# Kernel optimization log

Hardware: AMD Instinct MI355X
Metric: run time of the kernel (lower is better)

## Reference

```python
import jax, jax.numpy as jnp
import numpy as np

GRID = 128
N_PTS = 60000
K = 27


def _occupied_coords():
    # Deterministic blob-like occupancy: top-N voxels of a smooth random field.
    rng = np.random.RandomState(0)
    xs = np.arange(GRID, dtype=np.float32)
    X, Y, Z = np.meshgrid(xs, xs, xs, indexing='ij')
    f = np.zeros((GRID, GRID, GRID), np.float32)
    for _ in range(12):
        k = rng.uniform(0.04, 0.22, 3).astype(np.float32)
        ph = np.float32(rng.uniform(0, 2 * np.pi))
        a = np.float32(rng.randn())
        f += a * np.cos(k[0] * X + k[1] * Y + k[2] * Z + ph)
    idx = np.argpartition(f.ravel(), -N_PTS)[-N_PTS:]
    return np.stack(np.unravel_index(idx, f.shape), axis=1).astype(np.int64)


def _keys(c):
    return (c[:, 0] * GRID + c[:, 1]) * GRID + c[:, 2]


def _build_kmap(coords):
    # ME-style kernel map: for each of 27 offsets, pairs (input_row, output_row)
    # such that coord[out] + offset == coord[in]. Padded with index n (dummy row).
    n = coords.shape[0]
    key = _keys(coords)
    order = np.argsort(key)
    skey = key[order]
    ins, outs = [], []
    for dx in (-1, 0, 1):
        for dy in (-1, 0, 1):
            for dz in (-1, 0, 1):
                q = coords + np.array([dx, dy, dz], dtype=np.int64)
                valid = np.all((q >= 0) & (q < GRID), axis=1)
                qk = _keys(q)
                pos = np.clip(np.searchsorted(skey, qk), 0, n - 1)
                hit = valid & (skey[pos] == qk)
                ins.append(order[pos[hit]].astype(np.int32))
                outs.append(np.nonzero(hit)[0].astype(np.int32))
    m = max(len(a) for a in ins)
    in_idx = np.full((K, m), n, np.int32)
    out_idx = np.full((K, m), n, np.int32)
    for k in range(K):
        in_idx[k, : len(ins[k])] = ins[k]
        out_idx[k, : len(outs[k])] = outs[k]
    return jnp.asarray(in_idx), jnp.asarray(out_idx)


def setup_inputs() -> dict:
    coords = _occupied_coords()
    in1, out1 = _build_kmap(coords)
    pc, parent = np.unique(coords // 2, axis=0, return_inverse=True)  # maxpool k2 s2
    in2, out2 = _build_kmap(pc)
    n_pool = int(pc.shape[0])
    ks = jax.random.split(jax.random.key(0), 12)
    f32 = jnp.float32
    feats = jax.random.normal(ks[0], (N_PTS, 128), f32)
    W1 = jax.random.normal(ks[1], (K, 128, 128), f32) / np.sqrt(128 * K)
    W2 = jax.random.normal(ks[2], (K, 128, 256), f32) / np.sqrt(128 * K)
    W3 = jax.random.normal(ks[3], (K, 256, 256), f32) / np.sqrt(256 * K)
    W4 = jax.random.normal(ks[4], (K, 256, 256), f32) / np.sqrt(256 * K)
    g1 = 1.0 + 0.1 * jax.random.normal(ks[5], (128,), f32)
    b1 = 0.1 * jax.random.normal(ks[6], (128,), f32)
    g2 = 1.0 + 0.1 * jax.random.normal(ks[7], (256,), f32)
    b2 = 0.1 * jax.random.normal(ks[8], (256,), f32)
    g3 = 1.0 + 0.1 * jax.random.normal(ks[9], (256,), f32)
    b3 = 0.1 * jax.random.normal(ks[10], (256,), f32)
    return dict(feats=feats, W1=W1, g1=g1, b1=b1, W2=W2, g2=g2, b2=b2,
                W3=W3, g3=g3, b3=b3, W4=W4,
                in1=in1, out1=out1, in2=in2, out2=out2,
                parent=jnp.asarray(parent.astype(np.int32)), n_pool=n_pool)


def _sparse_conv(x, in_idx, out_idx, W, n_out):
    # x: [N_in, Cin]; in_idx/out_idx: [K, M] padded with N_in / n_out; W: [K, Cin, Cout]
    xp = jnp.concatenate([x, jnp.zeros((1, x.shape[1]), x.dtype)], axis=0)
    acc0 = jnp.zeros((n_out + 1, W.shape[2]), x.dtype)

    def step(acc, xs):
        i, o, Wk = xs
        return acc.at[o].add(xp[i] @ Wk), None

    acc, _ = jax.lax.scan(step, acc0, (in_idx, out_idx, W))
    return acc[:-1]


def _bn_relu(x, g, b):
    # training-mode BatchNorm over active voxels (ME applies BatchNorm1d to features)
    m = x.mean(0)
    v = x.var(0)
    return jax.nn.relu((x - m) * jax.lax.rsqrt(v + 1e-5) * g + b)


def reference(feats, W1, g1, b1, W2, g2, b2, W3, g3, b3, W4,
              in1, out1, in2, out2, parent, n_pool):
    n = feats.shape[0]
    x = _bn_relu(_sparse_conv(feats, in1, out1, W1, n), g1, b1)          # [N,128]
    x = jax.ops.segment_max(x, parent, num_segments=n_pool)             # maxpool 2x2x2/2
    x = _bn_relu(_sparse_conv(x, in2, out2, W2, n_pool), g2, b2)         # [Np,256]
    x = _bn_relu(_sparse_conv(x, in2, out2, W3, n_pool), g3, b3)         # [Np,256]
    return _sparse_conv(x, in2, out2, W4, n_pool)                        # [Np,256]
```

## Files before the change

### kernel.cpp

```cpp
#include <hip/hip_runtime.h>
#include <hip/hip_bf16.h>
#include <math.h>

#define K_OFF 27

typedef __attribute__((ext_vector_type(8))) short short8v;
typedef __attribute__((ext_vector_type(4))) float float4v;

static __device__ __forceinline__ unsigned short f2bf(float f) {
  __hip_bfloat16 h = __float2bfloat16(f);
  return *reinterpret_cast<unsigned short*>(&h);
}

static __device__ __forceinline__ void gload_lds16(const void* g, void* l) {
  __builtin_amdgcn_global_load_lds(
      (const __attribute__((address_space(1))) void*)g,
      (__attribute__((address_space(3))) void*)l, 16, 0, 0);
}

__global__ void fill_i32_kernel(int* __restrict__ p, int total, int val) {
  int i = blockIdx.x * blockDim.x + threadIdx.x;
  if (i < total) p[i] = val;
}

__global__ void build_table_kernel(const int* __restrict__ in_idx,
                                   const int* __restrict__ out_idx,
                                   int* __restrict__ table, int M, int n_valid,
                                   int n_out_pad) {
  int j = blockIdx.x * blockDim.x + threadIdx.x;
  if (j >= K_OFF * M) return;
  int k = j / M;
  int in = in_idx[j], out = out_idx[j];
  if (in < n_valid && out < n_valid) table[k * n_out_pad + out] = in;
}

__global__ void wtrans_kernel(const float* __restrict__ W,
                              unsigned short* __restrict__ Wt, int Cin,
                              int Cout) {
  __shared__ float t[32][33];
  const int k = blockIdx.z, ci0 = blockIdx.x * 32, co0 = blockIdx.y * 32;
  const float* Wk = W + (size_t)k * Cin * Cout;
  unsigned short* Wtk = Wt + (size_t)k * Cout * Cin;
#pragma unroll
  for (int i = 0; i < 4; ++i)
    t[threadIdx.y + i * 8][threadIdx.x] =
        Wk[(size_t)(ci0 + threadIdx.y + i * 8) * Cout + co0 + threadIdx.x];
  __syncthreads();
#pragma unroll
  for (int i = 0; i < 4; ++i)
    Wtk[(size_t)(co0 + threadIdx.y + i * 8) * Cin + ci0 + threadIdx.x] =
        f2bf(t[threadIdx.x][threadIdx.y + i * 8]);
}

__global__ void f32_to_bf16_kernel(const float* __restrict__ s,
                                   unsigned short* __restrict__ d, int total) {
  int i = (blockIdx.x * blockDim.x + threadIdx.x) * 4;
  if (i >= total) return;
  float4 v = *reinterpret_cast<const float4*>(s + i);
  ushort4 o = {f2bf(v.x), f2bf(v.y), f2bf(v.z), f2bf(v.w)};
  *reinterpret_cast<ushort4*>(d + i) = o;
}

template <int CIN, int KPG>
__global__ __launch_bounds__(256) void spconv_mfma(
    const unsigned short* __restrict__ xb,
    const unsigned short* __restrict__ Wt,
    const int* __restrict__ table,
    float* __restrict__ y, int n_out, int n_out_pad, int Cout) {
  constexpr int BK = 32;
  constexpr int SPK = CIN / BK;
  constexpr int S = KPG * SPK;

  __shared__ unsigned short As[2][128 * BK];
  __shared__ unsigned short Bs[2][128 * BK];
  __shared__ int idx_s[KPG * 128];

  const int tid = threadIdx.x;
  const int lane = tid & 63;
  const int wid = tid >> 6;
  const int row0 = blockIdx.x * 128;
  const int col0 = blockIdx.y * 128;
  const int kbase = blockIdx.z * KPG;
  const int wr = wid >> 1, wc = wid & 1;

  for (int j = tid; j < KPG * 128; j += 256)
    idx_s[j] = table[(kbase + (j >> 7)) * n_out_pad + row0 + (j & 127)];
  __syncthreads();

  const int srow = tid >> 2;
  const int sc4 = tid & 3;

  auto stage = [&](int buf, int s) {
    const int kl = s / SPK;
    const int kk0 = (s % SPK) * BK;
    const int* idk = &idx_s[kl << 7];
#pragma unroll
    for (int r = 0; r < 2; ++r) {
      const int row = r * 64 + srow;
      const int cg = sc4 ^ ((row >> 1) & 3);
      const int irow = idk[row];
      const unsigned short* srcA = xb + (size_t)irow * CIN + kk0 + cg * 8;
      gload_lds16(srcA, (void*)&As[buf][(r * 64 + wid * 16) * BK]);
      const unsigned short* srcB =
          Wt + ((size_t)(kbase + kl) * Cout + col0 + row) * CIN + kk0 + cg * 8;
      gload_lds16(srcB, (void*)&Bs[buf][(r * 64 + wid * 16) * BK]);
    }
  };

  int a_off[4], b_off[4];
#pragma unroll
  for (int mi = 0; mi < 4; ++mi) {
    const int row = wr * 64 + mi * 16 + (lane & 15);
    const int ca = (lane >> 4) ^ ((row >> 1) & 3);
    a_off[mi] = row * BK + ca * 8;
    const int rowb = wc * 64 + mi * 16 + (lane & 15);
    const int cb = (lane >> 4) ^ ((rowb >> 1) & 3);
    b_off[mi] = rowb * BK + cb * 8;
  }

  float4v acc[4][4];
#pragma unroll
  for (int i = 0; i < 4; ++i)
#pragma unroll
    for (int j = 0; j < 4; ++j) acc[i][j] = (float4v)(0.f);

  stage(0, 0);
  for (int s = 0; s < S; ++s) {
    const int buf = s & 1;
    __syncthreads();
    if (s + 1 < S) stage(buf ^ 1, s + 1);
    short8v a[4], b[4];
#pragma unroll
    for (int i = 0; i < 4; ++i) {
      a[i] = *reinterpret_cast<const short8v*>(&As[buf][a_off[i]]);
      b[i] = *reinterpret_cast<const short8v*>(&Bs[buf][b_off[i]]);
    }
#pragma unroll
    for (int mi = 0; mi < 4; ++mi)
#pragma unroll
      for (int ni = 0; ni < 4; ++ni)
        acc[mi][ni] = __builtin_amdgcn_mfma_f32_16x16x32_bf16(
            a[mi], b[ni], acc[mi][ni], 0, 0, 0);
  }

#pragma unroll
  for (int mi = 0; mi < 4; ++mi) {
    const int rbase = row0 + wr * 64 + mi * 16 + ((lane >> 4) << 2);
#pragma unroll
    for (int ni = 0; ni < 4; ++ni) {
      const int col = col0 + wc * 64 + ni * 16 + (lane & 15);
#pragma unroll
      for (int j = 0; j < 4; ++j) {
        const int r = rbase + j;
        if (r < n_out) atomicAdd(&y[(size_t)r * Cout + col], acc[mi][ni][j]);
      }
    }
  }
}

__global__ void colstats_kernel(const float* __restrict__ y, int n, int C,
                                double* __restrict__ sums) {
  const int c = threadIdx.x;
  const int r0 = blockIdx.x * 64;
  const int r1 = min(r0 + 64, n);
  double s = 0.0, s2 = 0.0;
  for (int r = r0; r < r1; ++r) {
    float v = y[(size_t)r * C + c];
    s += v;
    s2 += (double)v * (double)v;
  }
  atomicAdd(&sums[c], s);
  atomicAdd(&sums[C + c], s2);
}

__global__ void finalize_kernel(const double* __restrict__ sums,
                                const float* __restrict__ g,
                                const float* __restrict__ b,
                                float* __restrict__ scale,
                                float* __restrict__ shift, int n, int C) {
  int c = blockIdx.x * blockDim.x + threadIdx.x;
  if (c >= C) return;
  double m = sums[c] / n;
  double v = sums[C + c] / n - m * m;
  float sc = (float)((double)g[c] / sqrt(v + 1e-5));
  scale[c] = sc;
  shift[c] = b[c] - (float)m * sc;
}

__global__ void bn_relu_pool_kernel(const float* __restrict__ y,
                                    const float* __restrict__ scale,
                                    const float* __restrict__ shift,
                                    const int* __restrict__ parent,
                                    unsigned int* __restrict__ pooled, int n,
                                    int C) {
  int i4 = (blockIdx.x * blockDim.x + threadIdx.x) * 4;
  if (i4 >= n * C) return;
  int r = i4 / C, c = i4 % C;
  float4 v = *reinterpret_cast<const float4*>(y + i4);
  float4 sc = *reinterpret_cast<const float4*>(scale + c);
  float4 sh = *reinterpret_cast<const float4*>(shift + c);
  unsigned int* dst = pooled + (size_t)parent[r] * C + c;
  atomicMax(dst + 0, __float_as_uint(fmaxf(fmaf(v.x, sc.x, sh.x), 0.f)));
  atomicMax(dst + 1, __float_as_uint(fmaxf(fmaf(v.y, sc.y, sh.y), 0.f)));
  atomicMax(dst + 2, __float_as_uint(fmaxf(fmaf(v.z, sc.z, sh.z), 0.f)));
  atomicMax(dst + 3, __float_as_uint(fmaxf(fmaf(v.w, sc.w, sh.w), 0.f)));
}

__global__ void bn_relu_bf16_kernel(const float* __restrict__ y,
                                    const float* __restrict__ scale,
                                    const float* __restrict__ shift,
                                    unsigned short* __restrict__ xb, int total,
                                    int C) {
  int i4 = (blockIdx.x * blockDim.x + threadIdx.x) * 4;
  if (i4 >= total) return;
  int c = i4 % C;
  float4 v = *reinterpret_cast<const float4*>(y + i4);
  float4 sc = *reinterpret_cast<const float4*>(scale + c);
  float4 sh = *reinterpret_cast<const float4*>(shift + c);
  ushort4 o = {f2bf(fmaxf(fmaf(v.x, sc.x, sh.x), 0.f)),
               f2bf(fmaxf(fmaf(v.y, sc.y, sh.y), 0.f)),
               f2bf(fmaxf(fmaf(v.z, sc.z, sh.z), 0.f)),
               f2bf(fmaxf(fmaf(v.w, sc.w, sh.w), 0.f))};
  *reinterpret_cast<ushort4*>(xb + i4) = o;
}

extern "C" void kernel_launch(void* const* d_in, const int* in_sizes, int n_in_,
                              void* d_out, int out_size, void* d_ws,
                              size_t ws_size, hipStream_t stream) {
  const float* feats = (const float*)d_in[0];
  const float* W1 = (const float*)d_in[1];
  const float* g1 = (const float*)d_in[2];
  const float* b1 = (const float*)d_in[3];
  const float* W2 = (const float*)d_in[4];
  const float* g2 = (const float*)d_in[5];
  const float* b2 = (const float*)d_in[6];
  const float* W3 = (const float*)d_in[7];
  const float* g3 = (const float*)d_in[8];
  const float* b3 = (const float*)d_in[9];
  const float* W4 = (const float*)d_in[10];
  const int* in1 = (const int*)d_in[11];
  const int* out1 = (const int*)d_in[12];
  const int* in2 = (const int*)d_in[13];
  const int* out2 = (const int*)d_in[14];
  const int* parent = (const int*)d_in[15];

  const int N1 = in_sizes[0] / 128;
  const int M1 = in_sizes[11] / K_OFF;
  const int M2 = in_sizes[13] / K_OFF;
  const int NP = out_size / 256;

  const int n1_blocks = (N1 + 127) / 128, n1_pad = n1_blocks * 128;
  const int np_blocks = (NP + 127) / 128, np_pad = np_blocks * 128;

  auto rnd = [](size_t v) { return (v + 255) & ~size_t(255); };
  auto mx = [](size_t a, size_t b) { return a > b ? a : b; };
  char* ws = (char*)d_ws;
  size_t off = 0;
  auto take = [&](size_t b) { void* p = ws + off; off += rnd(b); return p; };

  const size_t sz_y1 = (size_t)N1 * 128 * 4;
  const size_t sz_y23 = (size_t)NP * 256 * 4;
  const size_t sz_x1 = ((size_t)N1 + 1) * 128 * 2;
  const size_t sz_x23 = ((size_t)NP + 1) * 256 * 2;
  const size_t sz_t1 = (size_t)K_OFF * n1_pad * 4;
  const size_t sz_t2 = (size_t)K_OFF * np_pad * 4;
  const size_t sz_pool = (size_t)NP * 128 * 4;
  const size_t sz_poolbf = ((size_t)NP + 1) * 128 * 2;
  const size_t sz_wt2 = (size_t)K_OFF * 128 * 256 * 2;
  const size_t sz_wt34 = (size_t)K_OFF * 256 * 256 * 2;

  char* A = (char*)take(mx(rnd(sz_y1), 2 * rnd(sz_y23)));
  float* y1 = (float*)A;
  float* y2 = (float*)A;
  float* y3 = (float*)(A + rnd(sz_y23));
  char* B = (char*)take(
      mx(rnd(sz_x1), rnd(sz_wt2) + 2 * rnd(sz_wt34) + rnd(sz_poolbf)));
  unsigned short* x1b = (unsigned short*)B;
  unsigned short* Wt2 = (unsigned short*)B;
  unsigned short* Wt3 = (unsigned short*)(B + rnd(sz_wt2));
  unsigned short* Wt4 = (unsigned short*)(B + rnd(sz_wt2) + rnd(sz_wt34));
  unsigned short* poolbf =
      (unsigned short*)(B + rnd(sz_wt2) + 2 * rnd(sz_wt34));
  char* C = (char*)take(mx(rnd(sz_t1), mx(rnd(sz_pool), rnd(sz_x23))));
  int* table1 = (int*)C;
  float* pooled = (float*)C;
  unsigned short* x2b = (unsigned short*)C;
  unsigned short* x3b = (unsigned short*)C;
  int* table2 = (int*)take(sz_t2);
  unsigned short* Wt1 = (unsigned short*)take((size_t)K_OFF * 128 * 128 * 2);
  double* sums = (double*)take(3 * 512 * 8);
  double* sums1 = sums; double* sums2 = sums + 512; double* sums3 = sums + 1024;
  float* scsh = (float*)take(6 * 256 * 4);
  float* sc1 = scsh;        float* sh1 = scsh + 256;
  float* sc2 = scsh + 512;  float* sh2 = scsh + 768;
  float* sc3 = scsh + 1024; float* sh3 = scsh + 1280;

  dim3 wtb(32, 8);
  wtrans_kernel<<<dim3(4, 4, K_OFF), wtb, 0, stream>>>(W1, Wt1, 128, 128);

  f32_to_bf16_kernel<<<(N1 * 128 / 4 + 255) / 256, 256, 0, stream>>>(
      feats, x1b, N1 * 128);
  hipMemsetAsync(x1b + (size_t)N1 * 128, 0, 128 * 2, stream);

  fill_i32_kernel<<<(K_OFF * n1_pad + 255) / 256, 256, 0, stream>>>(
      table1, K_OFF * n1_pad, N1);
  fill_i32_kernel<<<(K_OFF * np_pad + 255) / 256, 256, 0, stream>>>(
      table2, K_OFF * np_pad, NP);
  build_table_kernel<<<(K_OFF * M1 + 255) / 256, 256, 0, stream>>>(
      in1, out1, table1, M1, N1, n1_pad);
  build_table_kernel<<<(K_OFF * M2 + 255) / 256, 256, 0, stream>>>(
      in2, out2, table2, M2, NP, np_pad);
  hipMemsetAsync(sums, 0, 3 * 512 * 8, stream);

  hipMemsetAsync(y1, 0, sz_y1, stream);
  spconv_mfma<128, 9><<<dim3(n1_blocks, 1, 3), 256, 0, stream>>>(
      x1b, Wt1, table1, y1, N1, n1_pad, 128);
  colstats_kernel<<<(N1 + 63) / 64, 128, 0, stream>>>(y1, N1, 128, sums1);
  finalize_kernel<<<1, 128, 0, stream>>>(sums1, g1, b1, sc1, sh1, N1, 128);
  wtrans_kernel<<<dim3(4, 8, K_OFF), wtb, 0, stream>>>(W2, Wt2, 128, 256);
  wtrans_kernel<<<dim3(8, 8, K_OFF), wtb, 0, stream>>>(W3, Wt3, 256, 256);
  wtrans_kernel<<<dim3(8, 8, K_OFF), wtb, 0, stream>>>(W4, Wt4, 256, 256);
  hipMemsetAsync(pooled, 0, sz_pool, stream);
  bn_relu_pool_kernel<<<((N1 * 128 / 4) + 255) / 256, 256, 0, stream>>>(
      y1, sc1, sh1, parent, (unsigned int*)pooled, N1, 128);
  f32_to_bf16_kernel<<<((NP * 128 / 4) + 255) / 256, 256, 0, stream>>>(
      pooled, poolbf, NP * 128);
  hipMemsetAsync(poolbf + (size_t)NP * 128, 0, 128 * 2, stream);

  hipMemsetAsync(y2, 0, sz_y23, stream);
  spconv_mfma<128, 3><<<dim3(np_blocks, 2, 9), 256, 0, stream>>>(
      poolbf, Wt2, table2, y2, NP, np_pad, 256);
  colstats_kernel<<<(NP + 63) / 64, 256, 0, stream>>>(y2, NP, 256, sums2);
  finalize_kernel<<<1, 256, 0, stream>>>(sums2, g2, b2, sc2, sh2, NP, 256);
  bn_relu_bf16_kernel<<<((NP * 256 / 4) + 255) / 256, 256, 0, stream>>>(
      y2, sc2, sh2, x2b, NP * 256, 256);
  hipMemsetAsync(x2b + (size_t)NP * 256, 0, 256 * 2, stream);

  hipMemsetAsync(y3, 0, sz_y23, stream);
  spconv_mfma<256, 3><<<dim3(np_blocks, 2, 9), 256, 0, stream>>>(
      x2b, Wt3, table2, y3, NP, np_pad, 256);
  colstats_kernel<<<(NP + 63) / 64, 256, 0, stream>>>(y3, NP, 256, sums3);
  finalize_kernel<<<1, 256, 0, stream>>>(sums3, g3, b3, sc3, sh3, NP, 256);
  bn_relu_bf16_kernel<<<((NP * 256 / 4) + 255) / 256, 256, 0, stream>>>(
      y3, sc3, sh3, x3b, NP * 256, 256);
  hipMemsetAsync(x3b + (size_t)NP * 256, 0, 256 * 2, stream);

  hipMemsetAsync(d_out, 0, (size_t)out_size * 4, stream);
  spconv_mfma<256, 3><<<dim3(np_blocks, 2, 9), 256, 0, stream>>>(
      x3b, Wt4, table2, (float*)d_out, NP, np_pad, 256);
}
```

Baseline: 769.7 us.

## Replace atomic split-K accumulation with partial buffers and a fused reduce+stats pass

Each offset-group block now writes its partial result to a separate slice of a scratch buffer with plain stores instead of atomicAdd into a zeroed output. A new kernel sums the partial slices, writes the final output and computes the BatchNorm column statistics, replacing colstats and the output memsets. The goal is to avoid float atomic contention and the memset traffic. In exchange it needs a large extra workspace, up to 9x the output size, and adds a read pass over all partials. If the workspace is too small it falls back to the atomic path.

```diff
diff --git a/kernel.cpp b/kernel.cpp
--- a/kernel.cpp
+++ b/kernel.cpp
@@ -61,12 +61,13 @@
   *reinterpret_cast<ushort4*>(d + i) = o;
 }
 
-template <int CIN, int KPG>
+template <int CIN, int KPG, bool ATOMIC>
 __global__ __launch_bounds__(256) void spconv_mfma(
     const unsigned short* __restrict__ xb,
     const unsigned short* __restrict__ Wt,
     const int* __restrict__ table,
-    float* __restrict__ y, int n_out, int n_out_pad, int Cout) {
+    float* __restrict__ y, size_t gstride, int n_out, int n_out_pad,
+    int Cout) {
   constexpr int BK = 32;
   constexpr int SPK = CIN / BK;
   constexpr int S = KPG * SPK;
@@ -143,6 +144,7 @@
             a[mi], b[ni], acc[mi][ni], 0, 0, 0);
   }
 
+  float* yo = ATOMIC ? y : (y + (size_t)blockIdx.z * gstride);
 #pragma unroll
   for (int mi = 0; mi < 4; ++mi) {
     const int rbase = row0 + wr * 64 + mi * 16 + ((lane >> 4) << 2);
@@ -152,9 +154,35 @@
 #pragma unroll
       for (int j = 0; j < 4; ++j) {
         const int r = rbase + j;
-        if (r < n_out) atomicAdd(&y[(size_t)r * Cout + col], acc[mi][ni][j]);
+        if (r < n_out) {
+          if (ATOMIC)
+            atomicAdd(&yo[(size_t)r * Cout + col], acc[mi][ni][j]);
+          else
+            yo[(size_t)r * Cout + col] = acc[mi][ni][j];
+        }
       }
     }
+  }
+}
+
+__global__ void reduce_stats_kernel(const float* __restrict__ parts,
+                                    size_t gstride, int G,
+                                    float* __restrict__ y, int n, int C,
+                                    double* __restrict__ sums) {
+  const int c = threadIdx.x;
+  const int r0 = blockIdx.x * 64;
+  const int r1 = min(r0 + 64, n);
+  double s = 0.0, s2 = 0.0;
+  for (int r = r0; r < r1; ++r) {
+    float v = 0.f;
+    for (int g = 0; g < G; ++g) v += parts[g * gstride + (size_t)r * C + c];
+    y[(size_t)r * C + c] = v;
+    s += v;
+    s2 += (double)v * (double)v;
+  }
+  if (sums) {
+    atomicAdd(&sums[c], s);
+    atomicAdd(&sums[C + c], s2);
   }
 }
 
@@ -268,6 +296,10 @@
   const size_t sz_poolbf = ((size_t)NP + 1) * 128 * 2;
   const size_t sz_wt2 = (size_t)K_OFF * 128 * 256 * 2;
   const size_t sz_wt34 = (size_t)K_OFF * 256 * 256 * 2;
+
+  const size_t gs1 = (size_t)n1_pad * 128;
+  const size_t gs2 = (size_t)np_pad * 256;
+  const size_t sz_P = mx(3 * gs1 * 4, 9 * gs2 * 4);
 
   char* A = (char*)take(mx(rnd(sz_y1), 2 * rnd(sz_y23)));
   float* y1 = (float*)A;
@@ -294,6 +326,10 @@
   float* sc1 = scsh;        float* sh1 = scsh + 256;
   float* sc2 = scsh + 512;  float* sh2 = scsh + 768;
   float* sc3 = scsh + 1024; float* sh3 = scsh + 1280;
+  size_t off_noP = off;
+  float* P = (float*)take(sz_P);
+  const bool tierA = (off <= ws_size);
+  if (!tierA) off = off_noP;
 
   dim3 wtb(32, 8);
   wtrans_kernel<<<dim3(4, 4, K_OFF), wtb, 0, stream>>>(W1, Wt1, 128, 128);
@@ -312,10 +348,17 @@
       in2, out2, table2, M2, NP, np_pad);
   hipMemsetAsync(sums, 0, 3 * 512 * 8, stream);
 
-  hipMemsetAsync(y1, 0, sz_y1, stream);
-  spconv_mfma<128, 9><<<dim3(n1_blocks, 1, 3), 256, 0, stream>>>(
-      x1b, Wt1, table1, y1, N1, n1_pad, 128);
-  colstats_kernel<<<(N1 + 63) / 64, 128, 0, stream>>>(y1, N1, 128, sums1);
+  if (tierA) {
+    spconv_mfma<128, 9, false><<<dim3(n1_blocks, 1, 3), 256, 0, stream>>>(
+        x1b, Wt1, table1, P, gs1, N1, n1_pad, 128);
+    reduce_stats_kernel<<<(N1 + 63) / 64, 128, 0, stream>>>(
+        P, gs1, 3, y1, N1, 128, sums1);
+  } else {
+    hipMemsetAsync(y1, 0, sz_y1, stream);
+    spconv_mfma<128, 9, true><<<dim3(n1_blocks, 1, 3), 256, 0, stream>>>(
+        x1b, Wt1, table1, y1, 0, N1, n1_pad, 128);
+    colstats_kernel<<<(N1 + 63) / 64, 128, 0, stream>>>(y1, N1, 128, sums1);
+  }
   finalize_kernel<<<1, 128, 0, stream>>>(sums1, g1, b1, sc1, sh1, N1, 128);
   wtrans_kernel<<<dim3(4, 8, K_OFF), wtb, 0, stream>>>(W2, Wt2, 128, 256);
   wtrans_kernel<<<dim3(8, 8, K_OFF), wtb, 0, stream>>>(W3, Wt3, 256, 256);
@@ -327,25 +370,46 @@
       pooled, poolbf, NP * 128);
   hipMemsetAsync(poolbf + (size_t)NP * 128, 0, 128 * 2, stream);
 
-  hipMemsetAsync(y2, 0, sz_y23, stream);
-  spconv_mfma<128, 3><<<dim3(np_blocks, 2, 9), 256, 0, stream>>>(
-      poolbf, Wt2, table2, y2, NP, np_pad, 256);
-  colstats_kernel<<<(NP + 63) / 64, 256, 0, stream>>>(y2, NP, 256, sums2);
+  if (tierA) {
+    spconv_mfma<128, 3, false><<<dim3(np_blocks, 2, 9), 256, 0, stream>>>(
+        poolbf, Wt2, table2, P, gs2, NP, np_pad, 256);
+    reduce_stats_kernel<<<(NP + 63) / 64, 256, 0, stream>>>(
+        P, gs2, 9, y2, NP, 256, sums2);
+  } else {
+    hipMemsetAsync(y2, 0, sz_y23, stream);
+    spconv_mfma<128, 3, true><<<dim3(np_blocks, 2, 9), 256, 0, stream>>>(
+        poolbf, Wt2, table2, y2, 0, NP, np_pad, 256);
+    colstats_kernel<<<(NP + 63) / 64, 256, 0, stream>>>(y2, NP, 256, sums2);
+  }
   finalize_kernel<<<1, 256, 0, stream>>>(sums2, g2, b2, sc2, sh2, NP, 256);
   bn_relu_bf16_kernel<<<((NP * 256 / 4) + 255) / 256, 256, 0, stream>>>(
       y2, sc2, sh2, x2b, NP * 256, 256);
   hipMemsetAsync(x2b + (size_t)NP * 256, 0, 256 * 2, stream);
 
-  hipMemsetAsync(y3, 0, sz_y23, stream);
-  spconv_mfma<256, 3><<<dim3(np_blocks, 2, 9), 256, 0, stream>>>(
-      x2b, Wt3, table2, y3, NP, np_pad, 256);
-  colstats_kernel<<<(NP + 63) / 64, 256, 0, stream>>>(y3, NP, 256, sums3);
+  if (tierA) {
+    spconv_mfma<256, 3, false><<<dim3(np_blocks, 2, 9), 256, 0, stream>>>(
+        x2b, Wt3, table2, P, gs2, NP, np_pad, 256);
+    reduce_stats_kernel<<<(NP + 63) / 64, 256, 0, stream>>>(
+        P, gs2, 9, y3, NP, 256, sums3);
+  } else {
+    hipMemsetAsync(y3, 0, sz_y23, stream);
+    spconv_mfma<256, 3, true><<<dim3(np_blocks, 2, 9), 256, 0, stream>>>(
+        x2b, Wt3, table2, y3, 0, NP, np_pad, 256);
+    colstats_kernel<<<(NP + 63) / 64, 256, 0, stream>>>(y3, NP, 256, sums3);
+  }
   finalize_kernel<<<1, 256, 0, stream>>>(sums3, g3, b3, sc3, sh3, NP, 256);
   bn_relu_bf16_kernel<<<((NP * 256 / 4) + 255) / 256, 256, 0, stream>>>(
       y3, sc3, sh3, x3b, NP * 256, 256);
   hipMemsetAsync(x3b + (size_t)NP * 256, 0, 256 * 2, stream);
 
-  hipMemsetAsync(d_out, 0, (size_t)out_size * 4, stream);
-  spconv_mfma<256, 3><<<dim3(np_blocks, 2, 9), 256, 0, stream>>>(
-      x3b, Wt4, table2, (float*)d_out, NP, np_pad, 256);
-}
+  if (tierA) {
+    spconv_mfma<256, 3, false><<<dim3(np_blocks, 2, 9), 256, 0, stream>>>(
+        x3b, Wt4, table2, P, gs2, NP, np_pad, 256);
+    reduce_stats_kernel<<<(NP + 63) / 64, 256, 0, stream>>>(
+        P, gs2, 9, (float*)d_out, NP, 256, nullptr);
+  } else {
+    hipMemsetAsync(d_out, 0, (size_t)out_size * 4, stream);
+    spconv_mfma<256, 3, true><<<dim3(np_blocks, 2, 9), 256, 0, stream>>>(
+        x3b, Wt4, table2, (float*)d_out, 0, NP, np_pad, 256);
+  }
+}
```

Result: slower. 1.003 ms (+30.4%).
